# Kernel tuning notes

Measured on AMD Instinct MI355X. Metric: run time of the kernel, lower is better.

## Reference

```python
import jax, jax.numpy as jnp
import numpy as np

B = 8192            # batch.size
NNZ = B * 32        # active features per position ~32
FT = 512            # ft_out
F_FULL = 49152      # HalfKA feature count
F_VIRT = 768        # factorized (virtual) feature count


def setup_inputs() -> dict:
    key = jax.random.key(0)
    ks = jax.random.split(key, 8)
    s_ft = 1.0 / np.sqrt(F_FULL).astype(np.float32)
    s_fft = 1.0 / np.sqrt(F_VIRT).astype(np.float32)
    s_out = 1.0 / np.sqrt(2 * FT).astype(np.float32)
    return {
        "values": jnp.ones((NNZ,), dtype=jnp.float32),
        # W_ft stored feature-major [F_FULL, FT] = torch ft.weight.T, so rows are gathered per feature
        "W_ft": jax.random.uniform(ks[0], (F_FULL, FT), jnp.float32, -s_ft, s_ft),
        "ft_b": jax.random.uniform(ks[1], (FT,), jnp.float32, -s_ft, s_ft),
        "W_fft": jax.random.uniform(ks[2], (F_VIRT, FT), jnp.float32, -s_fft, s_fft),
        "fft_b": jax.random.uniform(ks[3], (FT,), jnp.float32, -s_fft, s_fft),
        "W_out": jax.random.uniform(ks[4], (1, 2 * FT), jnp.float32, -s_out, s_out),
        "out_b": jax.random.uniform(ks[5], (1,), jnp.float32, -s_out, s_out),
        "batch_ids": jnp.sort(jax.random.randint(ks[6], (NNZ,), 0, B)),
        "stm_feat": jax.random.randint(ks[7], (NNZ,), 0, F_FULL),
        "nstm_feat": jax.random.randint(jax.random.fold_in(key, 7), (NNZ,), 0, F_FULL),
        "size": B,
    }


def reference(values, W_ft, ft_b, W_fft, fft_b, W_out, out_b,
              batch_ids, stm_feat, nstm_feat, size):
    v = values[:, None]  # [NNZ, 1]

    def transform(feat):
        # sparse COO x dense weight == gather weight rows per active feature, scale, segment-sum
        acc = jax.ops.segment_sum(W_ft[feat] * v, batch_ids, num_segments=size)
        acc_v = jax.ops.segment_sum(W_fft[feat % F_VIRT] * v, batch_ids, num_segments=size)
        return acc + acc_v + ft_b + fft_b  # both Linear biases applied once per row

    stm_ft = transform(stm_feat)    # [B, FT]
    nstm_ft = transform(nstm_feat)  # [B, FT]
    hidden = jnp.clip(jnp.concatenate([stm_ft, nstm_ft], axis=1), 0.0, 1.0)
    return jax.nn.sigmoid(hidden @ W_out.T + out_b)  # [B, 1]
```

## Files before the change

kernel.cpp:

```cpp
#include <hip/hip_runtime.h>
#include <hip/hip_bf16.h>
#include <math.h>


constexpr int FT      = 512;
constexpr int FV      = 768;
constexpr int THREADS = 128;
constexpr int CHUNK   = 128;

__global__ __launch_bounds__(THREADS)
void nnue_kernel(const float* __restrict__ values,
                 const float* __restrict__ W_ft,
                 const float* __restrict__ ft_b,
                 const float* __restrict__ W_fft,
                 const float* __restrict__ fft_b,
                 const float* __restrict__ W_out,
                 const float* __restrict__ out_b,
                 const int*   __restrict__ batch_ids,
                 const int*   __restrict__ stm_feat,
                 const int*   __restrict__ nstm_feat,
                 int nnz,
                 float* __restrict__ out)
{
    const int b   = blockIdx.x;
    const int t   = threadIdx.x;
    const int col = t * 4;

    int lo0 = 0, hi0 = nnz;
    while (lo0 < hi0) {
        int mid = (lo0 + hi0) >> 1;
        if (batch_ids[mid] < b) lo0 = mid + 1; else hi0 = mid;
    }
    int lo1 = lo0, hi1 = nnz;
    while (lo1 < hi1) {
        int mid = (lo1 + hi1) >> 1;
        if (batch_ids[mid] < b + 1) lo1 = mid + 1; else hi1 = mid;
    }
    const int seg_lo = lo0, seg_hi = lo1;

    __shared__ int   sh_off_s [CHUNK];
    __shared__ int   sh_off_sv[CHUNK];
    __shared__ int   sh_off_n [CHUNK];
    __shared__ int   sh_off_nv[CHUNK];
    __shared__ float sh_v     [CHUNK];

    float4 acc_s = make_float4(0.f, 0.f, 0.f, 0.f);
    float4 acc_n = make_float4(0.f, 0.f, 0.f, 0.f);

    for (int base = seg_lo; base < seg_hi; base += CHUNK) {
        const int cnt = min(CHUNK, seg_hi - base);
        __syncthreads();
        if (t < cnt) {
            int fs = stm_feat[base + t];
            int fn = nstm_feat[base + t];
            sh_off_s [t] = fs * FT;
            sh_off_sv[t] = (fs % FV) * FT;
            sh_off_n [t] = fn * FT;
            sh_off_nv[t] = (fn % FV) * FT;
            sh_v     [t] = values[base + t];
        }
        __syncthreads();

        #pragma unroll 2
        for (int j = 0; j < cnt; ++j) {
            const int   os  = sh_off_s [j];
            const int   osv = sh_off_sv[j];
            const int   on  = sh_off_n [j];
            const int   onv = sh_off_nv[j];
            const float v   = sh_v[j];

            const float4 a  = *(const float4*)(W_ft  + os  + col);
            const float4 av = *(const float4*)(W_fft + osv + col);
            const float4 c  = *(const float4*)(W_ft  + on  + col);
            const float4 cv = *(const float4*)(W_fft + onv + col);

            acc_s.x = fmaf(a.x + av.x, v, acc_s.x);
            acc_s.y = fmaf(a.y + av.y, v, acc_s.y);
            acc_s.z = fmaf(a.z + av.z, v, acc_s.z);
            acc_s.w = fmaf(a.w + av.w, v, acc_s.w);
            acc_n.x = fmaf(c.x + cv.x, v, acc_n.x);
            acc_n.y = fmaf(c.y + cv.y, v, acc_n.y);
            acc_n.z = fmaf(c.z + cv.z, v, acc_n.z);
            acc_n.w = fmaf(c.w + cv.w, v, acc_n.w);
        }
    }

    const float4 fb  = *(const float4*)(ft_b  + col);
    const float4 vb  = *(const float4*)(fft_b + col);
    const float4 wos = *(const float4*)(W_out + col);
    const float4 won = *(const float4*)(W_out + FT + col);

    float partial = 0.f;
    {
        float h;
        h = fminf(fmaxf(acc_s.x + fb.x + vb.x, 0.f), 1.f); partial = fmaf(h, wos.x, partial);
        h = fminf(fmaxf(acc_s.y + fb.y + vb.y, 0.f), 1.f); partial = fmaf(h, wos.y, partial);
        h = fminf(fmaxf(acc_s.z + fb.z + vb.z, 0.f), 1.f); partial = fmaf(h, wos.z, partial);
        h = fminf(fmaxf(acc_s.w + fb.w + vb.w, 0.f), 1.f); partial = fmaf(h, wos.w, partial);
        h = fminf(fmaxf(acc_n.x + fb.x + vb.x, 0.f), 1.f); partial = fmaf(h, won.x, partial);
        h = fminf(fmaxf(acc_n.y + fb.y + vb.y, 0.f), 1.f); partial = fmaf(h, won.y, partial);
        h = fminf(fmaxf(acc_n.z + fb.z + vb.z, 0.f), 1.f); partial = fmaf(h, won.z, partial);
        h = fminf(fmaxf(acc_n.w + fb.w + vb.w, 0.f), 1.f); partial = fmaf(h, won.w, partial);
    }

    #pragma unroll
    for (int off = 32; off > 0; off >>= 1)
        partial += __shfl_down(partial, off, 64);

    __shared__ float wave_sum[THREADS / 64];
    if ((t & 63) == 0) wave_sum[t >> 6] = partial;
    __syncthreads();
    if (t == 0) {
        float s = wave_sum[0] + wave_sum[1] + out_b[0];
        out[b] = 1.0f / (1.0f + expf(-s));
    }
}

extern "C" void kernel_launch(void* const* d_in, const int* in_sizes, int n_in,
                              void* d_out, int out_size, void* d_ws, size_t ws_size,
                              hipStream_t stream) {
    const float* values    = (const float*)d_in[0];
    const float* W_ft      = (const float*)d_in[1];
    const float* ft_b      = (const float*)d_in[2];
    const float* W_fft     = (const float*)d_in[3];
    const float* fft_b     = (const float*)d_in[4];
    const float* W_out     = (const float*)d_in[5];
    const float* out_b     = (const float*)d_in[6];
    const int*   batch_ids = (const int*)d_in[7];
    const int*   stm_feat  = (const int*)d_in[8];
    const int*   nstm_feat = (const int*)d_in[9];

    const int nnz = in_sizes[0];
    const int B   = out_size;

    nnue_kernel<<<B, THREADS, 0, stream>>>(
        values, W_ft, ft_b, W_fft, fft_b, W_out, out_b,
        batch_ids, stm_feat, nstm_feat, nnz, (float*)d_out);
}
```

Measured before the change: 242.0 us.

## Split each row's nonzeros across two thread groups and unroll gathers by four

Doubles the block to 256 threads, with two 128-thread groups each handling alternate nonzeros of the same batch row. The partial accumulators are then combined through shared memory before the epilogue. The inner loop is also manually unrolled to issue sixteen float4 gathers at once, for more memory-level parallelism per thread. This costs more registers, an extra reduction step, and idle threads in the epilogue.

```diff
diff --git a/kernel.cpp b/kernel.cpp
--- a/kernel.cpp
+++ b/kernel.cpp
@@ -5,8 +5,8 @@
 
 constexpr int FT      = 512;
 constexpr int FV      = 768;
-constexpr int THREADS = 128;
-constexpr int CHUNK   = 128;
+constexpr int THREADS = 256;
+constexpr int CHUNK   = 256;
 
 __global__ __launch_bounds__(THREADS)
 void nnue_kernel(const float* __restrict__ values,
@@ -24,7 +24,9 @@
 {
     const int b   = blockIdx.x;
     const int t   = threadIdx.x;
-    const int col = t * 4;
+    const int g   = t >> 7;
+    const int lt  = t & 127;
+    const int col = lt * 4;
 
     int lo0 = 0, hi0 = nnz;
     while (lo0 < hi0) {
@@ -43,6 +45,8 @@
     __shared__ int   sh_off_n [CHUNK];
     __shared__ int   sh_off_nv[CHUNK];
     __shared__ float sh_v     [CHUNK];
+    __shared__ float4 sh_comb_s[FT / 4];
+    __shared__ float4 sh_comb_n[FT / 4];
 
     float4 acc_s = make_float4(0.f, 0.f, 0.f, 0.f);
     float4 acc_n = make_float4(0.f, 0.f, 0.f, 0.f);
@@ -61,37 +65,100 @@
         }
         __syncthreads();
 
-        #pragma unroll 2
-        for (int j = 0; j < cnt; ++j) {
-            const int   os  = sh_off_s [j];
-            const int   osv = sh_off_sv[j];
-            const int   on  = sh_off_n [j];
-            const int   onv = sh_off_nv[j];
-            const float v   = sh_v[j];
-
-            const float4 a  = *(const float4*)(W_ft  + os  + col);
-            const float4 av = *(const float4*)(W_fft + osv + col);
-            const float4 c  = *(const float4*)(W_ft  + on  + col);
-            const float4 cv = *(const float4*)(W_fft + onv + col);
-
-            acc_s.x = fmaf(a.x + av.x, v, acc_s.x);
-            acc_s.y = fmaf(a.y + av.y, v, acc_s.y);
-            acc_s.z = fmaf(a.z + av.z, v, acc_s.z);
-            acc_s.w = fmaf(a.w + av.w, v, acc_s.w);
-            acc_n.x = fmaf(c.x + cv.x, v, acc_n.x);
-            acc_n.y = fmaf(c.y + cv.y, v, acc_n.y);
-            acc_n.z = fmaf(c.z + cv.z, v, acc_n.z);
-            acc_n.w = fmaf(c.w + cv.w, v, acc_n.w);
+        int j = g;
+        for (; j + 6 < cnt; j += 8) {
+            const int j0 = j, j1 = j + 2, j2 = j + 4, j3 = j + 6;
+            const float v0 = sh_v[j0], v1 = sh_v[j1], v2 = sh_v[j2], v3 = sh_v[j3];
+
+            const float4 a0  = *(const float4*)(W_ft  + sh_off_s [j0] + col);
+            const float4 av0 = *(const float4*)(W_fft + sh_off_sv[j0] + col);
+            const float4 c0  = *(const float4*)(W_ft  + sh_off_n [j0] + col);
+            const float4 cv0 = *(const float4*)(W_fft + sh_off_nv[j0] + col);
+            const float4 a1  = *(const float4*)(W_ft  + sh_off_s [j1] + col);
+            const float4 av1 = *(const float4*)(W_fft + sh_off_sv[j1] + col);
+            const float4 c1  = *(const float4*)(W_ft  + sh_off_n [j1] + col);
+            const float4 cv1 = *(const float4*)(W_fft + sh_off_nv[j1] + col);
+            const float4 a2  = *(const float4*)(W_ft  + sh_off_s [j2] + col);
+            const float4 av2 = *(const float4*)(W_fft + sh_off_sv[j2] + col);
+            const float4 c2  = *(const float4*)(W_ft  + sh_off_n [j2] + col);
+            const float4 cv2 = *(const float4*)(W_fft + sh_off_nv[j2] + col);
+            const float4 a3  = *(const float4*)(W_ft  + sh_off_s [j3] + col);
+            const float4 av3 = *(const float4*)(W_fft + sh_off_sv[j3] + col);
+            const float4 c3  = *(const float4*)(W_ft  + sh_off_n [j3] + col);
+            const float4 cv3 = *(const float4*)(W_fft + sh_off_nv[j3] + col);
+
+            acc_s.x = fmaf(a0.x + av0.x, v0, acc_s.x);
+            acc_s.y = fmaf(a0.y + av0.y, v0, acc_s.y);
+            acc_s.z = fmaf(a0.z + av0.z, v0, acc_s.z);
+            acc_s.w = fmaf(a0.w + av0.w, v0, acc_s.w);
+            acc_n.x = fmaf(c0.x + cv0.x, v0, acc_n.x);
+            acc_n.y = fmaf(c0.y + cv0.y, v0, acc_n.y);
+            acc_n.z = fmaf(c0.z + cv0.z, v0, acc_n.z);
+            acc_n.w = fmaf(c0.w + cv0.w, v0, acc_n.w);
+
+            acc_s.x = fmaf(a1.x + av1.x, v1, acc_s.x);
+            acc_s.y = fmaf(a1.y + av1.y, v1, acc_s.y);
+            acc_s.z = fmaf(a1.z + av1.z, v1, acc_s.z);
+            acc_s.w = fmaf(a1.w + av1.w, v1, acc_s.w);
+            acc_n.x = fmaf(c1.x + cv1.x, v1, acc_n.x);
+            acc_n.y = fmaf(c1.y + cv1.y, v1, acc_n.y);
+            acc_n.z = fmaf(c1.z + cv1.z, v1, acc_n.z);
+            acc_n.w = fmaf(c1.w + cv1.w, v1, acc_n.w);
+
+            acc_s.x = fmaf(a2.x + av2.x, v2, acc_s.x);
+            acc_s.y = fmaf(a2.y + av2.y, v2, acc_s.y);
+            acc_s.z = fmaf(a2.z + av2.z, v2, acc_s.z);
+            acc_s.w = fmaf(a2.w + av2.w, v2, acc_s.w);
+            acc_n.x = fmaf(c2.x + cv2.x, v2, acc_n.x);
+            acc_n.y = fmaf(c2.y + cv2.y, v2, acc_n.y);
+            acc_n.z = fmaf(c2.z + cv2.z, v2, acc_n.z);
+            acc_n.w = fmaf(c2.w + cv2.w, v2, acc_n.w);
+
+            acc_s.x = fmaf(a3.x + av3.x, v3, acc_s.x);
+            acc_s.y = fmaf(a3.y + av3.y, v3, acc_s.y);
+            acc_s.z = fmaf(a3.z + av3.z, v3, acc_s.z);
+            acc_s.w = fmaf(a3.w + av3.w, v3, acc_s.w);
+            acc_n.x = fmaf(c3.x + cv3.x, v3, acc_n.x);
+            acc_n.y = fmaf(c3.y + cv3.y, v3, acc_n.y);
+            acc_n.z = fmaf(c3.z + cv3.z, v3, acc_n.z);
+            acc_n.w = fmaf(c3.w + cv3.w, v3, acc_n.w);
         }
-    }
-
-    const float4 fb  = *(const float4*)(ft_b  + col);
-    const float4 vb  = *(const float4*)(fft_b + col);
-    const float4 wos = *(const float4*)(W_out + col);
-    const float4 won = *(const float4*)(W_out + FT + col);
+        for (; j < cnt; j += 2) {
+            const float v0 = sh_v[j];
+            const float4 a  = *(const float4*)(W_ft  + sh_off_s [j] + col);
+            const float4 av = *(const float4*)(W_fft + sh_off_sv[j] + col);
+            const float4 c  = *(const float4*)(W_ft  + sh_off_n [j] + col);
+            const float4 cv = *(const float4*)(W_fft + sh_off_nv[j] + col);
+            acc_s.x = fmaf(a.x + av.x, v0, acc_s.x);
+            acc_s.y = fmaf(a.y + av.y, v0, acc_s.y);
+            acc_s.z = fmaf(a.z + av.z, v0, acc_s.z);
+            acc_s.w = fmaf(a.w + av.w, v0, acc_s.w);
+            acc_n.x = fmaf(c.x + cv.x, v0, acc_n.x);
+            acc_n.y = fmaf(c.y + cv.y, v0, acc_n.y);
+            acc_n.z = fmaf(c.z + cv.z, v0, acc_n.z);
+            acc_n.w = fmaf(c.w + cv.w, v0, acc_n.w);
+        }
+    }
+
+    __syncthreads();
+    if (g == 1) {
+        sh_comb_s[lt] = acc_s;
+        sh_comb_n[lt] = acc_n;
+    }
+    __syncthreads();
 
     float partial = 0.f;
-    {
+    if (g == 0) {
+        const float4 os = sh_comb_s[lt];
+        const float4 on = sh_comb_n[lt];
+        acc_s.x += os.x; acc_s.y += os.y; acc_s.z += os.z; acc_s.w += os.w;
+        acc_n.x += on.x; acc_n.y += on.y; acc_n.z += on.z; acc_n.w += on.w;
+
+        const float4 fb  = *(const float4*)(ft_b  + col);
+        const float4 vb  = *(const float4*)(fft_b + col);
+        const float4 wos = *(const float4*)(W_out + col);
+        const float4 won = *(const float4*)(W_out + FT + col);
+
         float h;
         h = fminf(fmaxf(acc_s.x + fb.x + vb.x, 0.f), 1.f); partial = fmaf(h, wos.x, partial);
         h = fminf(fmaxf(acc_s.y + fb.y + vb.y, 0.f), 1.f); partial = fmaf(h, wos.y, partial);
@@ -111,7 +178,7 @@
     if ((t & 63) == 0) wave_sum[t >> 6] = partial;
     __syncthreads();
     if (t == 0) {
-        float s = wave_sum[0] + wave_sum[1] + out_b[0];
+        float s = wave_sum[0] + wave_sum[1] + wave_sum[2] + wave_sum[3] + out_b[0];
         out[b] = 1.0f / (1.0f + expf(-s));
     }
 }
```

Result: slower. 267.8 us (+10.7%).

## Convert weights to bf16 in workspace and gather half-width rows per wave

Applied to the files above, without the earlier changes.

Adds a pre-pass kernel that converts W_ft and W_fft to bf16 in the workspace on every call. The main kernel then gathers 16-byte bf16 rows with 8 columns per lane. The two waves each take alternate features and combine their partial sums through shared memory. The goal is to halve the random-gather traffic, at the cost of a full read and write of the 100MB weight table every call and reduced precision. If the workspace is too small, it falls back to the fp32 kernel.

```diff
diff --git a/kernel.cpp b/kernel.cpp
--- a/kernel.cpp
+++ b/kernel.cpp
@@ -8,23 +8,55 @@
 constexpr int THREADS = 128;
 constexpr int CHUNK   = 128;
 
+typedef __attribute__((ext_vector_type(8))) unsigned short ushort8_t;
+
+__device__ inline unsigned short f2bf(float x) {
+    union { float f; unsigned int u; } v; v.f = x;
+    unsigned int r = v.u + 0x7FFFu + ((v.u >> 16) & 1u);
+    return (unsigned short)(r >> 16);
+}
+__device__ inline float bf2f(unsigned short s) {
+    union { unsigned int u; float f; } v; v.u = ((unsigned int)s) << 16;
+    return v.f;
+}
+
+__global__ __launch_bounds__(256)
+void convert_kernel(const float* __restrict__ W_ft, const float* __restrict__ W_fft,
+                    unsigned short* __restrict__ ft_bf, unsigned short* __restrict__ fft_bf,
+                    int n8_ft, int n8_total)
+{
+    int i = blockIdx.x * 256 + threadIdx.x;
+    if (i >= n8_total) return;
+    const float* src; unsigned short* dst; int base;
+    if (i < n8_ft) { src = W_ft;  dst = ft_bf;  base = i * 8; }
+    else           { src = W_fft; dst = fft_bf; base = (i - n8_ft) * 8; }
+    const float4 f0 = *(const float4*)(src + base);
+    const float4 f1 = *(const float4*)(src + base + 4);
+    ushort8_t u;
+    u[0] = f2bf(f0.x); u[1] = f2bf(f0.y); u[2] = f2bf(f0.z); u[3] = f2bf(f0.w);
+    u[4] = f2bf(f1.x); u[5] = f2bf(f1.y); u[6] = f2bf(f1.z); u[7] = f2bf(f1.w);
+    *(ushort8_t*)(dst + base) = u;
+}
+
 __global__ __launch_bounds__(THREADS)
-void nnue_kernel(const float* __restrict__ values,
-                 const float* __restrict__ W_ft,
-                 const float* __restrict__ ft_b,
-                 const float* __restrict__ W_fft,
-                 const float* __restrict__ fft_b,
-                 const float* __restrict__ W_out,
-                 const float* __restrict__ out_b,
-                 const int*   __restrict__ batch_ids,
-                 const int*   __restrict__ stm_feat,
-                 const int*   __restrict__ nstm_feat,
-                 int nnz,
-                 float* __restrict__ out)
+void nnue_bf16_kernel(const float* __restrict__ values,
+                      const unsigned short* __restrict__ Wft,
+                      const float* __restrict__ ft_b,
+                      const unsigned short* __restrict__ Wfft,
+                      const float* __restrict__ fft_b,
+                      const float* __restrict__ W_out,
+                      const float* __restrict__ out_b,
+                      const int*   __restrict__ batch_ids,
+                      const int*   __restrict__ stm_feat,
+                      const int*   __restrict__ nstm_feat,
+                      int nnz,
+                      float* __restrict__ out)
 {
-    const int b   = blockIdx.x;
-    const int t   = threadIdx.x;
-    const int col = t * 4;
+    const int b    = blockIdx.x;
+    const int t    = threadIdx.x;
+    const int w    = t >> 6;
+    const int lane = t & 63;
+    const int col  = lane * 8;
 
     int lo0 = 0, hi0 = nnz;
     while (lo0 < hi0) {
@@ -43,9 +75,10 @@
     __shared__ int   sh_off_n [CHUNK];
     __shared__ int   sh_off_nv[CHUNK];
     __shared__ float sh_v     [CHUNK];
-
-    float4 acc_s = make_float4(0.f, 0.f, 0.f, 0.f);
-    float4 acc_n = make_float4(0.f, 0.f, 0.f, 0.f);
+    __shared__ float sh_comb  [2][FT];
+
+    float acc_s[8] = {0,0,0,0,0,0,0,0};
+    float acc_n[8] = {0,0,0,0,0,0,0,0};
 
     for (int base = seg_lo; base < seg_hi; base += CHUNK) {
         const int cnt = min(CHUNK, seg_hi - base);
@@ -61,19 +94,130 @@
         }
         __syncthreads();
 
+        #pragma unroll 4
+        for (int j = w; j < cnt; j += 2) {
+            const float v = sh_v[j];
+            const ushort8_t a  = *(const ushort8_t*)(Wft  + sh_off_s [j] + col);
+            const ushort8_t av = *(const ushort8_t*)(Wfft + sh_off_sv[j] + col);
+            const ushort8_t c  = *(const ushort8_t*)(Wft  + sh_off_n [j] + col);
+            const ushort8_t cv = *(const ushort8_t*)(Wfft + sh_off_nv[j] + col);
+            #pragma unroll
+            for (int k = 0; k < 8; ++k) {
+                acc_s[k] = fmaf(bf2f(a[k]) + bf2f(av[k]), v, acc_s[k]);
+                acc_n[k] = fmaf(bf2f(c[k]) + bf2f(cv[k]), v, acc_n[k]);
+            }
+        }
+    }
+
+    __syncthreads();
+    if (w == 1) {
+        #pragma unroll
+        for (int k = 0; k < 8; ++k) {
+            sh_comb[0][col + k] = acc_s[k];
+            sh_comb[1][col + k] = acc_n[k];
+        }
+    }
+    __syncthreads();
+
+    if (w == 0) {
+        #pragma unroll
+        for (int k = 0; k < 8; ++k) {
+            acc_s[k] += sh_comb[0][col + k];
+            acc_n[k] += sh_comb[1][col + k];
+        }
+
+        const float4 fb0 = *(const float4*)(ft_b  + col);
+        const float4 fb1 = *(const float4*)(ft_b  + col + 4);
+        const float4 vb0 = *(const float4*)(fft_b + col);
+        const float4 vb1 = *(const float4*)(fft_b + col + 4);
+        const float4 ws0 = *(const float4*)(W_out + col);
+        const float4 ws1 = *(const float4*)(W_out + col + 4);
+        const float4 wn0 = *(const float4*)(W_out + FT + col);
+        const float4 wn1 = *(const float4*)(W_out + FT + col + 4);
+
+        const float bias[8] = { fb0.x + vb0.x, fb0.y + vb0.y, fb0.z + vb0.z, fb0.w + vb0.w,
+                                fb1.x + vb1.x, fb1.y + vb1.y, fb1.z + vb1.z, fb1.w + vb1.w };
+        const float wos[8]  = { ws0.x, ws0.y, ws0.z, ws0.w, ws1.x, ws1.y, ws1.z, ws1.w };
+        const float won[8]  = { wn0.x, wn0.y, wn0.z, wn0.w, wn1.x, wn1.y, wn1.z, wn1.w };
+
+        float partial = 0.f;
+        #pragma unroll
+        for (int k = 0; k < 8; ++k) {
+            float hs = fminf(fmaxf(acc_s[k] + bias[k], 0.f), 1.f);
+            float hn = fminf(fmaxf(acc_n[k] + bias[k], 0.f), 1.f);
+            partial = fmaf(hs, wos[k], partial);
+            partial = fmaf(hn, won[k], partial);
+        }
+
+        #pragma unroll
+        for (int off = 32; off > 0; off >>= 1)
+            partial += __shfl_down(partial, off, 64);
+
+        if (lane == 0)
+            out[b] = 1.0f / (1.0f + expf(-(partial + out_b[0])));
+    }
+}
+
+__global__ __launch_bounds__(THREADS)
+void nnue_f32_kernel(const float* __restrict__ values,
+                     const float* __restrict__ W_ft,
+                     const float* __restrict__ ft_b,
+                     const float* __restrict__ W_fft,
+                     const float* __restrict__ fft_b,
+                     const float* __restrict__ W_out,
+                     const float* __restrict__ out_b,
+                     const int*   __restrict__ batch_ids,
+                     const int*   __restrict__ stm_feat,
+                     const int*   __restrict__ nstm_feat,
+                     int nnz,
+                     float* __restrict__ out)
+{
+    const int b   = blockIdx.x;
+    const int t   = threadIdx.x;
+    const int col = t * 4;
+
+    int lo0 = 0, hi0 = nnz;
+    while (lo0 < hi0) {
+        int mid = (lo0 + hi0) >> 1;
+        if (batch_ids[mid] < b) lo0 = mid + 1; else hi0 = mid;
+    }
+    int lo1 = lo0, hi1 = nnz;
+    while (lo1 < hi1) {
+        int mid = (lo1 + hi1) >> 1;
+        if (batch_ids[mid] < b + 1) lo1 = mid + 1; else hi1 = mid;
+    }
+    const int seg_lo = lo0, seg_hi = lo1;
+
+    __shared__ int   sh_off_s [CHUNK];
+    __shared__ int   sh_off_sv[CHUNK];
+    __shared__ int   sh_off_n [CHUNK];
+    __shared__ int   sh_off_nv[CHUNK];
+    __shared__ float sh_v     [CHUNK];
+
+    float4 acc_s = make_float4(0.f, 0.f, 0.f, 0.f);
+    float4 acc_n = make_float4(0.f, 0.f, 0.f, 0.f);
+
+    for (int base = seg_lo; base < seg_hi; base += CHUNK) {
+        const int cnt = min(CHUNK, seg_hi - base);
+        __syncthreads();
+        if (t < cnt) {
+            int fs = stm_feat[base + t];
+            int fn = nstm_feat[base + t];
+            sh_off_s [t] = fs * FT;
+            sh_off_sv[t] = (fs % FV) * FT;
+            sh_off_n [t] = fn * FT;
+            sh_off_nv[t] = (fn % FV) * FT;
+            sh_v     [t] = values[base + t];
+        }
+        __syncthreads();
+
         #pragma unroll 2
         for (int j = 0; j < cnt; ++j) {
-            const int   os  = sh_off_s [j];
-            const int   osv = sh_off_sv[j];
-            const int   on  = sh_off_n [j];
-            const int   onv = sh_off_nv[j];
-            const float v   = sh_v[j];
-
-            const float4 a  = *(const float4*)(W_ft  + os  + col);
-            const float4 av = *(const float4*)(W_fft + osv + col);
-            const float4 c  = *(const float4*)(W_ft  + on  + col);
-            const float4 cv = *(const float4*)(W_fft + onv + col);
-
+            const float v = sh_v[j];
+            const float4 a  = *(const float4*)(W_ft  + sh_off_s [j] + col);
+            const float4 av = *(const float4*)(W_fft + sh_off_sv[j] + col);
+            const float4 c  = *(const float4*)(W_ft  + sh_off_n [j] + col);
+            const float4 cv = *(const float4*)(W_fft + sh_off_nv[j] + col);
             acc_s.x = fmaf(a.x + av.x, v, acc_s.x);
             acc_s.y = fmaf(a.y + av.y, v, acc_s.y);
             acc_s.z = fmaf(a.z + av.z, v, acc_s.z);
@@ -130,10 +274,27 @@
     const int*   stm_feat  = (const int*)d_in[8];
     const int*   nstm_feat = (const int*)d_in[9];
 
-    const int nnz = in_sizes[0];
-    const int B   = out_size;
-
-    nnue_kernel<<<B, THREADS, 0, stream>>>(
-        values, W_ft, ft_b, W_fft, fft_b, W_out, out_b,
-        batch_ids, stm_feat, nstm_feat, nnz, (float*)d_out);
-}
+    const int nnz    = in_sizes[0];
+    const int B      = out_size;
+    const int n_ft   = in_sizes[1];
+    const int n_fft  = in_sizes[3];
+
+    const size_t need = (size_t)(n_ft + n_fft) * sizeof(unsigned short);
+
+    if (ws_size >= need) {
+        unsigned short* ft_bf  = (unsigned short*)d_ws;
+        unsigned short* fft_bf = ft_bf + n_ft;
+        const int n8_ft    = n_ft / 8;
+        const int n8_total = (n_ft + n_fft) / 8;
+        const int cgrid    = (n8_total + 255) / 256;
+        convert_kernel<<<cgrid, 256, 0, stream>>>(W_ft, W_fft, ft_bf, fft_bf,
+                                                  n8_ft, n8_total);
+        nnue_bf16_kernel<<<B, THREADS, 0, stream>>>(
+            values, ft_bf, ft_b, fft_bf, fft_b, W_out, out_b,
+            batch_ids, stm_feat, nstm_feat, nnz, (float*)d_out);
+    } else {
+        nnue_f32_kernel<<<B, THREADS, 0, stream>>>(
+            values, W_ft, ft_b, W_fft, fft_b, W_out, out_b,
+            batch_ids, stm_feat, nstm_feat, nnz, (float*)d_out);
+    }
+}
```

After: 236.7 us. -2.2%, faster.
